# Performance work log

Hardware: AMD Instinct MI355X
Metric: run time of the kernel (lower is better)

The kernel has to match this reference:

```python
import jax, jax.numpy as jnp
import numpy as np

B, T, D = 2, 4096, 1024          # batch, seq_len, d_model
L, H, F, K = 2, 16, 4096, 2048   # n_blocks, n_heads, d_ff, router top-k (T//2)
DH = D // H


def _ln(x, scale, bias):
    m = jnp.mean(x, -1, keepdims=True)
    v = jnp.var(x, -1, keepdims=True)
    return (x - m) * jax.lax.rsqrt(v + 1e-5) * scale + bias


def setup_inputs() -> dict:
    key = jax.random.key(0)
    ks = jax.random.split(key, 6)
    n = lambda k, sh, s: jax.random.normal(k, sh, jnp.float32) * s
    return {
        "x": n(ks[0], (B, T, D), 1.0),
        "w_router": n(ks[1], (D,), 0.02),
        "b_router": jnp.zeros((), jnp.float32),
        "ln1_scale": jnp.ones((L, D), jnp.float32),
        "ln1_bias": jnp.zeros((L, D), jnp.float32),
        "w_qkv": n(ks[2], (L, D, 3 * D), 0.02),
        "b_qkv": jnp.zeros((L, 3 * D), jnp.float32),
        "w_o": n(ks[3], (L, D, D), 0.02),
        "b_o": jnp.zeros((L, D), jnp.float32),
        "ln2_scale": jnp.ones((L, D), jnp.float32),
        "ln2_bias": jnp.zeros((L, D), jnp.float32),
        "w1": n(ks[4], (L, D, F), 0.02),
        "b1": jnp.zeros((L, F), jnp.float32),
        "w2": n(ks[5], (L, F, D), 0.02),
        "b2": jnp.zeros((L, D), jnp.float32),
    }


def reference(x, w_router, b_router, ln1_scale, ln1_bias, w_qkv, b_qkv,
              w_o, b_o, ln2_scale, ln2_bias, w1, b1, w2, b2):
    # 1. router scores all (active) tokens; prev_selected is None (first recursion step)
    logits = jnp.einsum('btd,d->bt', x, w_router) + b_router          # (B, T)
    # 2. expert-choice: top-K tokens by score
    _, idx = jax.lax.top_k(logits, K)                                  # (B, K)
    idx = jnp.sort(idx, axis=1)                                        # restore sequence order
    gate = jax.nn.sigmoid(jnp.take_along_axis(logits, idx, axis=1))[..., None]  # (B, K, 1)
    h = jnp.take_along_axis(x, idx[..., None], axis=1)                 # gather -> (B, K, D)
    # 3. shared transformer blocks on the gathered subsequence
    causal = jnp.tril(jnp.ones((K, K), bool))
    scale = 1.0 / np.sqrt(DH).astype(np.float32)
    for l in range(L):
        a = _ln(h, ln1_scale[l], ln1_bias[l])
        qkv = a @ w_qkv[l] + b_qkv[l]
        q, k_, v = jnp.split(qkv, 3, axis=-1)
        q = q.reshape(B, K, H, DH).transpose(0, 2, 1, 3)
        k_ = k_.reshape(B, K, H, DH).transpose(0, 2, 1, 3)
        v = v.reshape(B, K, H, DH).transpose(0, 2, 1, 3)
        s = jnp.einsum('bhqd,bhkd->bhqk', q, k_) * scale               # (B, H, K, K)
        s = jnp.where(causal, s, jnp.finfo(s.dtype).min)
        p = jax.nn.softmax(s, axis=-1)
        o = jnp.einsum('bhqk,bhkd->bhqd', p, v).transpose(0, 2, 1, 3).reshape(B, K, D)
        h = h + o @ w_o[l] + b_o[l]
        m = _ln(h, ln2_scale[l], ln2_bias[l])
        h = h + jax.nn.gelu(m @ w1[l] + b1[l]) @ w2[l] + b2[l]
    # 4. gate-weighted scatter-add back into the full hidden state
    h_out = h * gate
    total = x.at[jnp.arange(B)[:, None], idx].add(h_out)               # (B, T, D)
    return total, idx, logits
```

## Files before the change

kernel.cpp:

```cpp
#include <hip/hip_runtime.h>
#include <hip/hip_bf16.h>
#include <cstdint>

typedef unsigned short u16;
typedef __attribute__((ext_vector_type(8))) short s16x8;
typedef __attribute__((ext_vector_type(4))) float f32x4;
typedef __attribute__((ext_vector_type(4))) u16 u16x4;

constexpr int Bc = 2, Tc = 4096, Dc = 1024, Lc = 2, Hc = 16, Fc = 4096, Kc = 2048, DHc = 64;
constexpr int Mc = Bc * Kc;

__device__ __forceinline__ u16 f2b(float f) {
  __hip_bfloat16 h = __float2bfloat16(f);
  return *reinterpret_cast<u16*>(&h);
}

__device__ __forceinline__ float wred_sum(float v) {
#pragma unroll
  for (int m = 32; m >= 1; m >>= 1) v += __shfl_xor(v, m, 64);
  return v;
}

__device__ __forceinline__ void gl2lds16(const void* g, void* l) {
  __builtin_amdgcn_global_load_lds(
      (const __attribute__((address_space(1))) void*)(uintptr_t)g,
      (__attribute__((address_space(3))) void*)(uintptr_t)l, 16, 0, 0);
}

__global__ void transp_kernel(const float* __restrict__ in, u16* __restrict__ out, int R, int C) {
  __shared__ float t[32][33];
  int c0 = blockIdx.x * 32, r0 = blockIdx.y * 32;
  int tr = threadIdx.x >> 5, tc = threadIdx.x & 31;
#pragma unroll
  for (int i = 0; i < 4; i++)
    t[tr + i * 8][tc] = in[(size_t)(r0 + tr + i * 8) * C + c0 + tc];
  __syncthreads();
#pragma unroll
  for (int i = 0; i < 4; i++)
    out[(size_t)(c0 + tr + i * 8) * R + r0 + tc] = f2b(t[tc][tr + i * 8]);
}

__global__ void router_kernel(const float* __restrict__ x, const float* __restrict__ wr,
                              const float* __restrict__ br, float* __restrict__ out_lg,
                              float* __restrict__ ws_lg) {
  int tid = threadIdx.x, w = tid >> 6, l = tid & 63;
  int token = blockIdx.x * 4 + w;
  const float4* xr = (const float4*)(x + (size_t)token * Dc);
  const float4* wv = (const float4*)wr;
  float acc = 0.f;
#pragma unroll
  for (int i = 0; i < 4; i++) {
    float4 a = xr[l + i * 64], bw = wv[l + i * 64];
    acc += a.x * bw.x + a.y * bw.y + a.z * bw.z + a.w * bw.w;
  }
  acc = wred_sum(acc);
  if (l == 0) {
    float v = acc + br[0];
    out_lg[token] = v;
    ws_lg[token] = v;
  }
}

__global__ void topk_kernel(const float* __restrict__ logits, int* __restrict__ idxi,
                            float* __restrict__ gate, int* __restrict__ inv,
                            float* __restrict__ out_idx) {
  __shared__ float lg[Tc];
  __shared__ unsigned int key[Tc];
  __shared__ unsigned int hist[256];
  __shared__ unsigned int sscan[256];
  __shared__ unsigned int wsum[16], woff[16];
  __shared__ unsigned int sel_info[2];
  int b = blockIdx.x, tid = threadIdx.x;
#pragma unroll
  for (int j = 0; j < 4; j++) {
    int t = tid + j * 1024;
    float v = logits[b * Tc + t];
    lg[t] = v;
    unsigned int u = __float_as_uint(v);
    key[t] = (u & 0x80000000u) ? ~u : (u | 0x80000000u);
  }
  if (tid == 0) { sel_info[0] = 0u; sel_info[1] = (unsigned int)Kc; }
  __syncthreads();
  for (int pass = 0; pass < 4; ++pass) {
    int shift = 24 - 8 * pass;
    if (tid < 256) hist[tid] = 0u;
    __syncthreads();
    unsigned int prefix = sel_info[0];
#pragma unroll
    for (int j = 0; j < 4; j++) {
      unsigned int k = key[tid + j * 1024];
      if ((unsigned int)(((unsigned long long)k) >> (shift + 8)) == prefix)
        atomicAdd(&hist[(k >> shift) & 255u], 1u);
    }
    __syncthreads();
    if (tid < 256) sscan[tid] = hist[tid];
    __syncthreads();
    for (int s = 1; s < 256; s <<= 1) {
      unsigned int add = 0u;
      if (tid < 256 && tid + s < 256) add = sscan[tid + s];
      __syncthreads();
      if (tid < 256) sscan[tid] += add;
      __syncthreads();
    }
    if (tid < 256) {
      unsigned int above = sscan[tid] - hist[tid];
      unsigned int rem = sel_info[1];
      if (above < rem && sscan[tid] >= rem) {
        sel_info[0] = (prefix << 8) | (unsigned int)tid;
        sel_info[1] = rem - above;
      }
    }
    __syncthreads();
  }
  unsigned int thr = sel_info[0];
  unsigned int R = sel_info[1];
  int base = tid * 4;
  unsigned int sgt = 0, seq = 0;
#pragma unroll
  for (int j = 0; j < 4; j++) {
    unsigned int k = key[base + j];
    sgt += (k > thr); seq += (k == thr);
  }
  unsigned int pk = (sgt << 16) | seq;
  int lane = tid & 63, wid = tid >> 6;
  unsigned int inc = pk;
#pragma unroll
  for (int m = 1; m < 64; m <<= 1) {
    unsigned int o = __shfl_up(inc, m, 64);
    if (lane >= m) inc += o;
  }
  if (lane == 63) wsum[wid] = inc;
  __syncthreads();
  if (tid == 0) {
    unsigned int run = 0;
    for (int i2 = 0; i2 < 16; i2++) { woff[i2] = run; run += wsum[i2]; }
  }
  __syncthreads();
  unsigned int exc = inc - pk + woff[wid];
  unsigned int run_gt = exc >> 16, run_eq = exc & 0xFFFFu;
#pragma unroll
  for (int j = 0; j < 4; j++) {
    int t = base + j;
    unsigned int k = key[t];
    bool isgt = k > thr, iseq = (k == thr);
    bool selv = isgt || (iseq && run_eq < R);
    if (selv) {
      unsigned int pos = run_gt + (run_eq < R ? run_eq : R);
      idxi[b * Kc + pos] = t;
      out_idx[b * Kc + pos] = (float)t;
      gate[b * Kc + pos] = 1.f / (1.f + __expf(-lg[t]));
      inv[b * Tc + t] = (int)pos;
    } else {
      inv[b * Tc + t] = -1;
    }
    run_gt += isgt ? 1u : 0u;
    run_eq += iseq ? 1u : 0u;
  }
}

__global__ void gather_kernel(const float* __restrict__ x, const int* __restrict__ idxi,
                              float* __restrict__ h) {
  int blk = blockIdx.x, tid = threadIdx.x;
  int b = blk >> 11;
  int t = idxi[blk];
  ((float4*)(h + (size_t)blk * Dc))[tid] =
      ((const float4*)(x + ((size_t)b * Tc + t) * Dc))[tid];
}

__global__ void ln_kernel(const float* __restrict__ h, const float* __restrict__ sc,
                          const float* __restrict__ bi, u16* __restrict__ out) {
  __shared__ float red[8];
  int row = blockIdx.x, tid = threadIdx.x, w = tid >> 6, l = tid & 63;
  float4 v = ((const float4*)(h + (size_t)row * Dc))[tid];
  float s = v.x + v.y + v.z + v.w;
  float q = v.x * v.x + v.y * v.y + v.z * v.z + v.w * v.w;
  s = wred_sum(s);
  q = wred_sum(q);
  if (l == 0) { red[w] = s; red[w + 4] = q; }
  __syncthreads();
  s = red[0] + red[1] + red[2] + red[3];
  q = red[4] + red[5] + red[6] + red[7];
  float mean = s * (1.f / Dc);
  float var = q * (1.f / Dc) - mean * mean;
  float rsd = rsqrtf(var + 1e-5f);
  float4 scv = ((const float4*)sc)[tid];
  float4 biv = ((const float4*)bi)[tid];
  u16x4 o;
  o.x = f2b((v.x - mean) * rsd * scv.x + biv.x);
  o.y = f2b((v.y - mean) * rsd * scv.y + biv.y);
  o.z = f2b((v.z - mean) * rsd * scv.z + biv.z);
  o.w = f2b((v.w - mean) * rsd * scv.w + biv.w);
  *(u16x4*)(out + (size_t)row * Dc + tid * 4) = o;
}

template <int EPI>
__global__ void gemm_bt(const u16* __restrict__ A, const u16* __restrict__ BT,
                        const float* __restrict__ bias, int Kd, int N,
                        float* __restrict__ outf, u16* __restrict__ outb,
                        u16* __restrict__ qd, u16* __restrict__ kd, u16* __restrict__ vd) {
  __shared__ __align__(16) u16 lsA[128 * 32];
  __shared__ __align__(16) u16 lsB[128 * 32];
  int tid = threadIdx.x;
  int w = tid >> 6, l = tid & 63;
  int wu = __builtin_amdgcn_readfirstlane(w);
  int wr = w >> 1, wc = w & 1;
  int lr = l & 15, lg = l >> 4;
  int bm = blockIdx.y, bn = blockIdx.x;
  int srow = tid >> 2, scol = (tid & 3) * 8;
  const u16* ga = A + (size_t)(bm * 128 + srow) * Kd + scol;
  const u16* gb = BT + (size_t)(bn * 128 + srow) * Kd + scol;
  u16* la = lsA + wu * 512;
  u16* lb = lsB + wu * 512;
  f32x4 acc[4][4] = {};
  for (int kt = 0; kt < Kd; kt += 32) {
    gl2lds16(ga + kt, la);
    gl2lds16(ga + (size_t)64 * Kd + kt, la + 2048);
    gl2lds16(gb + kt, lb);
    gl2lds16(gb + (size_t)64 * Kd + kt, lb + 2048);
    __syncthreads();
    s16x8 af[4], bf[4];
#pragma unroll
    for (int i = 0; i < 4; i++)
      af[i] = *(const s16x8*)&lsA[(wr * 64 + i * 16 + lr) * 32 + lg * 8];
#pragma unroll
    for (int j = 0; j < 4; j++)
      bf[j] = *(const s16x8*)&lsB[(wc * 64 + j * 16 + lr) * 32 + lg * 8];
#pragma unroll
    for (int i = 0; i < 4; i++)
#pragma unroll
      for (int j = 0; j < 4; j++)
        acc[i][j] = __builtin_amdgcn_mfma_f32_16x16x32_bf16(af[i], bf[j], acc[i][j], 0, 0, 0);
    __syncthreads();
  }
  int row0 = bm * 128 + wr * 64 + lg * 4;
  int col0 = bn * 128 + wc * 64 + lr;
#pragma unroll
  for (int i = 0; i < 4; i++) {
#pragma unroll
    for (int j = 0; j < 4; j++) {
      int col = col0 + j * 16;
      float bcol = bias[col];
#pragma unroll
      for (int r = 0; r < 4; r++) {
        int row = row0 + i * 16 + r;
        float v = acc[i][j][r] + bcol;
        if constexpr (EPI == 0) {
          int sec = col >> 10, n1 = col & 1023, hh = n1 >> 6, dh = n1 & 63;
          int b = row >> 11, kq = row & 2047;
          size_t bh = (size_t)(b * Hc + hh);
          if (sec == 0) {
            qd[(bh * Kc + kq) * DHc + dh] = f2b(v * 0.125f);
          } else if (sec == 1) {
            kd[(bh * Kc + kq) * DHc + dh] = f2b(v);
          } else {
            vd[(bh * DHc + dh) * Kc + kq] = f2b(v);
          }
        } else if constexpr (EPI == 1) {
          outf[(size_t)row * N + col] += v;
        } else {
          float z = 0.7978845608028654f * (v + 0.044715f * v * v * v);
          float g = v / (1.f + __expf(-2.f * z));
          outb[(size_t)row * N + col] = f2b(g);
        }
      }
    }
  }
}

__global__ __launch_bounds__(256) void attn_fwd(const u16* __restrict__ Q,
                                                const u16* __restrict__ Kb,
                                                const u16* __restrict__ Vt,
                                                u16* __restrict__ O) {
  __shared__ __align__(16) u16 Kl[2][4096];
  __shared__ __align__(16) u16 Vl[2][4096];
  __shared__ __align__(16) u16 Pl[4][1024];
  int tid = threadIdx.x, w = tid >> 6, l = tid & 63;
  int lr = l & 15, lg = l >> 4;
  int bid = blockIdx.x;
  int qb = 31 - (bid >> 5);
  int bh = bid & 31;
  const u16* Qp = Q + (size_t)bh * Kc * DHc;
  const u16* Kp = Kb + (size_t)bh * Kc * DHc;
  const u16* Vp = Vt + (size_t)bh * DHc * Kc;
  int q0 = qb * 64 + w * 16;
  s16x8 qf0 = *(const s16x8*)(Qp + (size_t)(q0 + lr) * DHc + lg * 8);
  s16x8 qf1 = *(const s16x8*)(Qp + (size_t)(q0 + lr) * DHc + 32 + lg * 8);
  int skv = tid >> 2;
  int sc8 = (tid & 3) * 8;
  u16* pw = Pl[w];
  f32x4 oa[4] = {};
  float lsum[4] = {0.f, 0.f, 0.f, 0.f};

  auto stage = [&](int buf, int kv0) {
    const u16* kbase = Kp + (size_t)(kv0 + skv) * DHc + sc8;
    gl2lds16(kbase, &Kl[buf][w * 512]);
    gl2lds16(kbase + 32, &Kl[buf][2048 + w * 512]);
    const u16* vbase = Vp + (size_t)skv * Kc + kv0 + sc8;
    gl2lds16(vbase, &Vl[buf][w * 512]);
    gl2lds16(vbase + 32, &Vl[buf][2048 + w * 512]);
  };

  int nsteps = qb + 1;
  stage(0, 0);
  for (int t = 0; t < nsteps; ++t) {
    int cur = t & 1;
    int kv0 = t * 64;
    if (t + 1 < nsteps) {
      stage(cur ^ 1, kv0 + 64);
      asm volatile("s_waitcnt vmcnt(4)" ::: "memory");
    } else {
      asm volatile("s_waitcnt vmcnt(0)" ::: "memory");
    }
    __builtin_amdgcn_s_barrier();
    asm volatile("" ::: "memory");
    f32x4 s[4];
#pragma unroll
    for (int f = 0; f < 4; f++) {
      f32x4 z = {};
      z = __builtin_amdgcn_mfma_f32_16x16x32_bf16(
          qf0, *(const s16x8*)&Kl[cur][(f * 16 + lr) * 32 + lg * 8], z, 0, 0, 0);
      s[f] = __builtin_amdgcn_mfma_f32_16x16x32_bf16(
          qf1, *(const s16x8*)&Kl[cur][2048 + (f * 16 + lr) * 32 + lg * 8], z, 0, 0, 0);
    }
#pragma unroll
    for (int f = 0; f < 4; f++) {
      int kv = kv0 + f * 16 + lr;
#pragma unroll
      for (int r = 0; r < 4; r++) {
        int qrow = q0 + lg * 4 + r;
        float p = (kv <= qrow) ? __expf(s[f][r]) : 0.f;
        lsum[r] += p;
        pw[(f >> 1) * 512 + (lg * 4 + r) * 32 + (f & 1) * 16 + lr] = f2b(p);
      }
    }
#pragma unroll
    for (int ks = 0; ks < 2; ks++) {
      s16x8 pf = *(const s16x8*)&pw[ks * 512 + lr * 32 + lg * 8];
#pragma unroll
      for (int d4 = 0; d4 < 4; d4++)
        oa[d4] = __builtin_amdgcn_mfma_f32_16x16x32_bf16(
            pf, *(const s16x8*)&Vl[cur][ks * 2048 + (d4 * 16 + lr) * 32 + lg * 8],
            oa[d4], 0, 0, 0);
    }
    asm volatile("" ::: "memory");
    __builtin_amdgcn_s_barrier();
  }
#pragma unroll
  for (int msk = 1; msk < 16; msk <<= 1)
#pragma unroll
    for (int r = 0; r < 4; r++) lsum[r] += __shfl_xor(lsum[r], msk, 64);
  int b = bh >> 4, hh = bh & 15;
#pragma unroll
  for (int r = 0; r < 4; r++) {
    float invl = 1.f / lsum[r];
    int qrow = q0 + lg * 4 + r;
    u16* orow = O + ((size_t)(b * Kc + qrow) * Dc) + hh * DHc;
#pragma unroll
    for (int d4 = 0; d4 < 4; d4++)
      orow[d4 * 16 + lr] = f2b(oa[d4][r] * invl);
  }
}

__global__ void scatter_kernel(const float* __restrict__ x, const float* __restrict__ h,
                               const float* __restrict__ gate, const int* __restrict__ inv,
                               float* __restrict__ out) {
  int row = blockIdx.x, tid = threadIdx.x;
  int b = row >> 12;
  float4 xv = ((const float4*)(x + (size_t)row * Dc))[tid];
  int pos = inv[row];
  if (pos >= 0) {
    float g = gate[b * Kc + pos];
    float4 hv = ((const float4*)(h + (size_t)(b * Kc + pos) * Dc))[tid];
    xv.x += g * hv.x; xv.y += g * hv.y; xv.z += g * hv.z; xv.w += g * hv.w;
  }
  ((float4*)(out + (size_t)row * Dc))[tid] = xv;
}

extern "C" void kernel_launch(void* const* d_in, const int* in_sizes, int n_in,
                              void* d_out, int out_size, void* d_ws, size_t ws_size,
                              hipStream_t stream) {
  const float* x = (const float*)d_in[0];
  const float* w_router = (const float*)d_in[1];
  const float* b_router = (const float*)d_in[2];
  const float* ln1_s = (const float*)d_in[3];
  const float* ln1_b = (const float*)d_in[4];
  const float* w_qkv = (const float*)d_in[5];
  const float* b_qkv = (const float*)d_in[6];
  const float* w_o = (const float*)d_in[7];
  const float* b_o = (const float*)d_in[8];
  const float* ln2_s = (const float*)d_in[9];
  const float* ln2_b = (const float*)d_in[10];
  const float* w1 = (const float*)d_in[11];
  const float* b1 = (const float*)d_in[12];
  const float* w2 = (const float*)d_in[13];
  const float* b2 = (const float*)d_in[14];

  float* out_total = (float*)d_out;
  float* out_idx = out_total + (size_t)Bc * Tc * Dc;
  float* out_lg = out_idx + Bc * Kc;

  char* p = (char*)d_ws;
  auto carve = [&](size_t bytes) {
    char* r = p;
    p += (bytes + 255) & ~(size_t)255;
    return r;
  };
  float* lg_ws = (float*)carve((size_t)Bc * Tc * 4);
  int* idx_ws = (int*)carve((size_t)Bc * Kc * 4);
  float* gate_ws = (float*)carve((size_t)Bc * Kc * 4);
  int* inv_ws = (int*)carve((size_t)Bc * Tc * 4);
  float* h_ws = (float*)carve((size_t)Mc * Dc * 4);
  u16* a_bf = (u16*)carve((size_t)Mc * Dc * 2);
  u16* o_bf = (u16*)carve((size_t)Mc * Dc * 2);
  u16* g_bf = (u16*)carve((size_t)Mc * Fc * 2);
  u16* qbuf = (u16*)carve((size_t)Bc * Hc * Kc * DHc * 2);
  u16* kbuf = (u16*)carve((size_t)Bc * Hc * Kc * DHc * 2);
  u16* vtbuf = (u16*)carve((size_t)Bc * Hc * Kc * DHc * 2);
  u16* wqkvT = (u16*)carve((size_t)Lc * 3 * Dc * Dc * 2);
  u16* woT = (u16*)carve((size_t)Lc * Dc * Dc * 2);
  u16* w1T = (u16*)carve((size_t)Lc * Dc * Fc * 2);
  u16* w2T = (u16*)carve((size_t)Lc * Fc * Dc * 2);

  for (int l2 = 0; l2 < Lc; ++l2) {
    transp_kernel<<<dim3(3 * Dc / 32, Dc / 32), 256, 0, stream>>>(
        w_qkv + (size_t)l2 * Dc * 3 * Dc, wqkvT + (size_t)l2 * 3 * Dc * Dc, Dc, 3 * Dc);
    transp_kernel<<<dim3(Dc / 32, Dc / 32), 256, 0, stream>>>(
        w_o + (size_t)l2 * Dc * Dc, woT + (size_t)l2 * Dc * Dc, Dc, Dc);
    transp_kernel<<<dim3(Fc / 32, Dc / 32), 256, 0, stream>>>(
        w1 + (size_t)l2 * Dc * Fc, w1T + (size_t)l2 * Fc * Dc, Dc, Fc);
    transp_kernel<<<dim3(Dc / 32, Fc / 32), 256, 0, stream>>>(
        w2 + (size_t)l2 * Fc * Dc, w2T + (size_t)l2 * Dc * Fc, Fc, Dc);
  }
  router_kernel<<<Bc * Tc / 4, 256, 0, stream>>>(x, w_router, b_router, out_lg, lg_ws);
  topk_kernel<<<Bc, 1024, 0, stream>>>(lg_ws, idx_ws, gate_ws, inv_ws, out_idx);
  gather_kernel<<<Mc, 256, 0, stream>>>(x, idx_ws, h_ws);
  for (int l2 = 0; l2 < Lc; ++l2) {
    ln_kernel<<<Mc, 256, 0, stream>>>(h_ws, ln1_s + l2 * Dc, ln1_b + l2 * Dc, a_bf);
    gemm_bt<0><<<dim3(3 * Dc / 128, Mc / 128), 256, 0, stream>>>(
        a_bf, wqkvT + (size_t)l2 * 3 * Dc * Dc, b_qkv + l2 * 3 * Dc, Dc, 3 * Dc,
        nullptr, nullptr, qbuf, kbuf, vtbuf);
    attn_fwd<<<Bc * Hc * (Kc / 64), 256, 0, stream>>>(qbuf, kbuf, vtbuf, o_bf);
    gemm_bt<1><<<dim3(Dc / 128, Mc / 128), 256, 0, stream>>>(
        o_bf, woT + (size_t)l2 * Dc * Dc, b_o + l2 * Dc, Dc, Dc,
        h_ws, nullptr, nullptr, nullptr, nullptr);
    ln_kernel<<<Mc, 256, 0, stream>>>(h_ws, ln2_s + l2 * Dc, ln2_b + l2 * Dc, a_bf);
    gemm_bt<2><<<dim3(Fc / 128, Mc / 128), 256, 0, stream>>>(
        a_bf, w1T + (size_t)l2 * Fc * Dc, b1 + l2 * Fc, Dc, Fc,
        nullptr, g_bf, nullptr, nullptr, nullptr);
    gemm_bt<1><<<dim3(Dc / 128, Mc / 128), 256, 0, stream>>>(
        g_bf, w2T + (size_t)l2 * Dc * Fc, b2 + l2 * Dc, Fc, Dc,
        h_ws, nullptr, nullptr, nullptr, nullptr);
  }
  scatter_kernel<<<Bc * Tc, 256, 0, stream>>>(x, h_ws, gate_ws, inv_ws, out_total);
}
```

Baseline: 765.5 us.

## Double-buffer GEMM LDS loads, add XCD-aware block remap and split-K for narrow GEMMs

```diff
diff --git a/kernel.cpp b/kernel.cpp
--- a/kernel.cpp
+++ b/kernel.cpp
@@ -194,52 +194,74 @@
 }
 
 template <int EPI>
-__global__ void gemm_bt(const u16* __restrict__ A, const u16* __restrict__ BT,
-                        const float* __restrict__ bias, int Kd, int N,
-                        float* __restrict__ outf, u16* __restrict__ outb,
-                        u16* __restrict__ qd, u16* __restrict__ kd, u16* __restrict__ vd) {
-  __shared__ __align__(16) u16 lsA[128 * 32];
-  __shared__ __align__(16) u16 lsB[128 * 32];
+__global__ __launch_bounds__(256) void gemm_bt(
+    const u16* __restrict__ A, const u16* __restrict__ BT,
+    const float* __restrict__ bias, int Kd, int kdchunk, int N, int gridN,
+    float* __restrict__ outf, u16* __restrict__ outb,
+    u16* __restrict__ qd, u16* __restrict__ kd, u16* __restrict__ vd) {
+  __shared__ __align__(16) u16 lsA[2][128 * 32];
+  __shared__ __align__(16) u16 lsB[2][128 * 32];
   int tid = threadIdx.x;
   int w = tid >> 6, l = tid & 63;
   int wu = __builtin_amdgcn_readfirstlane(w);
   int wr = w >> 1, wc = w & 1;
   int lr = l & 15, lg = l >> 4;
-  int bm = blockIdx.y, bn = blockIdx.x;
+  int nwg = gridDim.x;
+  int orig = blockIdx.x;
+  int qq = nwg >> 3, rr = nwg & 7;
+  int xcd = orig & 7;
+  int wgid = (xcd < rr ? xcd * (qq + 1) : rr * (qq + 1) + (xcd - rr) * qq) + (orig >> 3);
+  int bm = wgid / gridN, bn = wgid % gridN;
+  int kz = blockIdx.z;
+  int k0 = kz * kdchunk;
   int srow = tid >> 2, scol = (tid & 3) * 8;
-  const u16* ga = A + (size_t)(bm * 128 + srow) * Kd + scol;
-  const u16* gb = BT + (size_t)(bn * 128 + srow) * Kd + scol;
-  u16* la = lsA + wu * 512;
-  u16* lb = lsB + wu * 512;
+  const u16* ga = A + (size_t)(bm * 128 + srow) * Kd + k0 + scol;
+  const u16* gb = BT + (size_t)(bn * 128 + srow) * Kd + k0 + scol;
+
+  auto stage = [&](int buf, int kt) {
+    gl2lds16(ga + kt, &lsA[buf][wu * 512]);
+    gl2lds16(ga + (size_t)64 * Kd + kt, &lsA[buf][2048 + wu * 512]);
+    gl2lds16(gb + kt, &lsB[buf][wu * 512]);
+    gl2lds16(gb + (size_t)64 * Kd + kt, &lsB[buf][2048 + wu * 512]);
+  };
+
   f32x4 acc[4][4] = {};
-  for (int kt = 0; kt < Kd; kt += 32) {
-    gl2lds16(ga + kt, la);
-    gl2lds16(ga + (size_t)64 * Kd + kt, la + 2048);
-    gl2lds16(gb + kt, lb);
-    gl2lds16(gb + (size_t)64 * Kd + kt, lb + 2048);
-    __syncthreads();
+  int nt = kdchunk >> 5;
+  stage(0, 0);
+  for (int t = 0; t < nt; ++t) {
+    int cur = t & 1;
+    if (t + 1 < nt) {
+      stage(cur ^ 1, (t + 1) * 32);
+      asm volatile("s_waitcnt vmcnt(4)" ::: "memory");
+    } else {
+      asm volatile("s_waitcnt vmcnt(0)" ::: "memory");
+    }
+    __builtin_amdgcn_s_barrier();
+    asm volatile("" ::: "memory");
     s16x8 af[4], bf[4];
 #pragma unroll
     for (int i = 0; i < 4; i++)
-      af[i] = *(const s16x8*)&lsA[(wr * 64 + i * 16 + lr) * 32 + lg * 8];
+      af[i] = *(const s16x8*)&lsA[cur][(wr * 64 + i * 16 + lr) * 32 + lg * 8];
 #pragma unroll
     for (int j = 0; j < 4; j++)
-      bf[j] = *(const s16x8*)&lsB[(wc * 64 + j * 16 + lr) * 32 + lg * 8];
+      bf[j] = *(const s16x8*)&lsB[cur][(wc * 64 + j * 16 + lr) * 32 + lg * 8];
 #pragma unroll
     for (int i = 0; i < 4; i++)
 #pragma unroll
       for (int j = 0; j < 4; j++)
         acc[i][j] = __builtin_amdgcn_mfma_f32_16x16x32_bf16(af[i], bf[j], acc[i][j], 0, 0, 0);
-    __syncthreads();
+    asm volatile("" ::: "memory");
+    __builtin_amdgcn_s_barrier();
   }
   int row0 = bm * 128 + wr * 64 + lg * 4;
   int col0 = bn * 128 + wc * 64 + lr;
+  bool addb = (kz == 0);
 #pragma unroll
   for (int i = 0; i < 4; i++) {
 #pragma unroll
     for (int j = 0; j < 4; j++) {
       int col = col0 + j * 16;
-      float bcol = bias[col];
+      float bcol = addb ? bias[col] : 0.f;
 #pragma unroll
       for (int r = 0; r < 4; r++) {
         int row = row0 + i * 16 + r;
@@ -256,7 +278,7 @@
             vd[(bh * DHc + dh) * Kc + kq] = f2b(v);
           }
         } else if constexpr (EPI == 1) {
-          outf[(size_t)row * N + col] += v;
+          atomicAdd(&outf[(size_t)row * N + col], v);
         } else {
           float z = 0.7978845608028654f * (v + 0.044715f * v * v * v);
           float g = v / (1.f + __expf(-2.f * z));
@@ -436,20 +458,20 @@
   gather_kernel<<<Mc, 256, 0, stream>>>(x, idx_ws, h_ws);
   for (int l2 = 0; l2 < Lc; ++l2) {
     ln_kernel<<<Mc, 256, 0, stream>>>(h_ws, ln1_s + l2 * Dc, ln1_b + l2 * Dc, a_bf);
-    gemm_bt<0><<<dim3(3 * Dc / 128, Mc / 128), 256, 0, stream>>>(
-        a_bf, wqkvT + (size_t)l2 * 3 * Dc * Dc, b_qkv + l2 * 3 * Dc, Dc, 3 * Dc,
-        nullptr, nullptr, qbuf, kbuf, vtbuf);
+    gemm_bt<0><<<dim3((3 * Dc / 128) * (Mc / 128), 1, 1), 256, 0, stream>>>(
+        a_bf, wqkvT + (size_t)l2 * 3 * Dc * Dc, b_qkv + l2 * 3 * Dc,
+        Dc, Dc, 3 * Dc, 3 * Dc / 128, nullptr, nullptr, qbuf, kbuf, vtbuf);
     attn_fwd<<<Bc * Hc * (Kc / 64), 256, 0, stream>>>(qbuf, kbuf, vtbuf, o_bf);
-    gemm_bt<1><<<dim3(Dc / 128, Mc / 128), 256, 0, stream>>>(
-        o_bf, woT + (size_t)l2 * Dc * Dc, b_o + l2 * Dc, Dc, Dc,
-        h_ws, nullptr, nullptr, nullptr, nullptr);
+    gemm_bt<1><<<dim3((Dc / 128) * (Mc / 128), 1, 2), 256, 0, stream>>>(
+        o_bf, woT + (size_t)l2 * Dc * Dc, b_o + l2 * Dc,
+        Dc, Dc / 2, Dc, Dc / 128, h_ws, nullptr, nullptr, nullptr, nullptr);
     ln_kernel<<<Mc, 256, 0, stream>>>(h_ws, ln2_s + l2 * Dc, ln2_b + l2 * Dc, a_bf);
-    gemm_bt<2><<<dim3(Fc / 128, Mc / 128), 256, 0, stream>>>(
-        a_bf, w1T + (size_t)l2 * Fc * Dc, b1 + l2 * Fc, Dc, Fc,
-        nullptr, g_bf, nullptr, nullptr, nullptr);
-    gemm_bt<1><<<dim3(Dc / 128, Mc / 128), 256, 0, stream>>>(
-        g_bf, w2T + (size_t)l2 * Dc * Fc, b2 + l2 * Dc, Fc, Dc,
-        h_ws, nullptr, nullptr, nullptr, nullptr);
+    gemm_bt<2><<<dim3((Fc / 128) * (Mc / 128), 1, 1), 256, 0, stream>>>(
+        a_bf, w1T + (size_t)l2 * Fc * Dc, b1 + l2 * Fc,
+        Dc, Dc, Fc, Fc / 128, nullptr, g_bf, nullptr, nullptr, nullptr);
+    gemm_bt<1><<<dim3((Dc / 128) * (Mc / 128), 1, 4), 256, 0, stream>>>(
+        g_bf, w2T + (size_t)l2 * Dc * Fc, b2 + l2 * Dc,
+        Fc, Fc / 4, Dc, Dc / 128, h_ws, nullptr, nullptr, nullptr, nullptr);
   }
   scatter_kernel<<<Bc * Tc, 256, 0, stream>>>(x, h_ws, gate_ws, inv_ws, out_total);
 }
```

New measurement: 746.3 us. 1.03x faster.
